# Optimization experiments

Measured on AMD Instinct MI355X. Metric: run time of the kernel, lower is better.

The kernel has to match this reference:

```python
import jax, jax.numpy as jnp
import numpy as np

N = 50000        # nodes
E = 800000       # edges
F_IN = 128       # dataset.num_features (== dim*heads so all conv layers share in_channels)
DIM = 32         # mParams['dim']
HEADS = 4        # mParams['num_heads']
HC = DIM * HEADS # 128
DEPTH = 2        # mParams['c_depth'] -> total conv layers = DEPTH + 1 = 3
L = DEPTH + 1
DIM2 = 16        # ceil(DIM/2)
NCLS = 6
SLOPE = 0.2      # GATv2Conv default negative_slope


def setup_inputs() -> dict:
    key = jax.random.key(0)
    ks = jax.random.split(key, 20)
    def lin(k, fan_in, shape):
        return jax.random.normal(k, shape, dtype=jnp.float32) / np.sqrt(fan_in)
    x = jax.random.normal(ks[0], (N, F_IN), dtype=jnp.float32)
    edge_index = jax.random.randint(ks[1], (2, E), 0, N, dtype=jnp.int64)
    batch = jnp.zeros((N,), dtype=jnp.int64)
    # stacked GATv2Conv params (all layers have in_channels = 128)
    Wl = lin(ks[2], F_IN, (L, F_IN, HC))   # lin_l weight (source transform)
    Wr = lin(ks[3], F_IN, (L, F_IN, HC))   # lin_r weight (target transform)
    bl = jnp.zeros((L, HC), dtype=jnp.float32)
    br = jnp.zeros((L, HC), dtype=jnp.float32)
    att = lin(ks[4], DIM, (L, HEADS, DIM)) # attention vector a
    cb = jnp.zeros((L, HC), dtype=jnp.float32)  # conv output bias
    W1 = lin(ks[5], HC, (HC, DIM));   b1 = jnp.zeros((DIM,), jnp.float32)
    W2 = lin(ks[6], DIM, (DIM, DIM2)); b2 = jnp.zeros((DIM2,), jnp.float32)
    W3 = lin(ks[7], 2 * DIM2, (2 * DIM2, NCLS)); b3 = jnp.zeros((NCLS,), jnp.float32)
    return {"x": x, "edge_index": edge_index, "batch": batch,
            "Wl": Wl, "Wr": Wr, "bl": bl, "br": br, "att": att, "cb": cb,
            "W1": W1, "b1": b1, "W2": W2, "b2": b2, "W3": W3, "b3": b3}


def _gatv2_layer(h, src, dst, Wl, Wr, bl, br, att, cb):
    # h: [N, F]; src/dst: [Ea] (self-loops included)
    xl = (h @ Wl + bl).reshape(N, HEADS, DIM)  # source-side transform
    xr = (h @ Wr + br).reshape(N, HEADS, DIM)  # target-side transform
    msg = xl[src] + xr[dst]                    # [Ea, H, C]
    e = jnp.where(msg > 0, msg, SLOPE * msg)   # leaky_relu
    score = jnp.einsum('ehc,hc->eh', e, att)   # [Ea, H]
    # scatter-softmax over destination nodes
    m = jax.ops.segment_max(score, dst, num_segments=N)        # [N, H]
    ex = jnp.exp(score - m[dst])
    s = jax.ops.segment_sum(ex, dst, num_segments=N)           # [N, H]
    alpha = ex / (s[dst] + 1e-16)                              # [Ea, H]
    out = jax.ops.segment_sum(alpha[:, :, None] * xl[src], dst, num_segments=N)
    return out.reshape(N, HC) + cb


def reference(x, edge_index, batch, Wl, Wr, bl, br, att, cb, W1, b1, W2, b2, W3, b3):
    src0, dst0 = edge_index[0], edge_index[1]
    loop = jnp.arange(N, dtype=edge_index.dtype)
    src = jnp.concatenate([src0, loop])  # GATv2Conv add_self_loops=True
    dst = jnp.concatenate([dst0, loop])
    h = x
    for i in range(L):
        h = jax.nn.relu(_gatv2_layer(h, src, dst, Wl[i], Wr[i], bl[i], br[i], att[i], cb[i]))
    h = jax.nn.relu(h @ W1 + b1)
    h = jax.nn.relu(h @ W2 + b2)
    # dropout(p=0.5) is identity in eval mode
    e = jnp.concatenate([h[src0], h[dst0]], axis=1)  # [E, 2*DIM2]
    out = e @ W3 + b3                                # [E, NCLS]
    return (out, e)
```

## Files before the change

kernel.cpp:

```cpp
#include <hip/hip_runtime.h>
#include <hip/hip_bf16.h>

typedef __hip_bfloat16 bf16;
typedef __attribute__((ext_vector_type(8))) short bf16x8;
typedef __attribute__((ext_vector_type(4))) float f32x4;

#define N_NODES 50000
#define E_EDGES 800000
#define EA (E_EDGES + N_NODES)
#define HC 128
#define HEADS 4
#define DIM 32
#define DIM2 16
#define NCLS 6
#define SLOPE 0.2f
#define XN (N_NODES * HC)
#define GM 32
#define HSTRIDE 152
#define WSWZ_L 32768
#define NCHUNK ((N_NODES + 1023) / 1024)

#define P_CVTI (2 * E_EDGES)
#define P_PRM  6390
#define P_WSWZ (3 * WSWZ_L)
#define P_TOT  (P_CVTI + P_PRM + P_WSWZ)

__device__ __forceinline__ float b2f(bf16 v) { return __bfloat162float(v); }
__device__ __forceinline__ unsigned short f2bfu(float f) {
    bf16 b = __float2bfloat16(f);
    return *(unsigned short*)&b;
}
__device__ __forceinline__ unsigned packbf(float a, float b) {
    return (unsigned)f2bfu(a) | ((unsigned)f2bfu(b) << 16);
}

__device__ __forceinline__ void block_detect(const void* wptr, const void* eptr,
                                             int* det, int& isf32, int& is64) {
    int tid = threadIdx.x;
    if (tid == 0) { det[0] = 0; det[1] = 0; }
    __syncthreads();
    const unsigned short* w = (const unsigned short*)wptr;
    int badf = 0;
    for (int i = tid; i < 1024; i += 256) {
        unsigned v = w[i];
        unsigned ex = (v >> 7) & 0xFF;
        if (v != 0 && (ex < 90 || ex > 150)) badf++;
    }
    const int* ei = (const int*)eptr;
    int nz = 0;
    for (int i = tid; i < 1024; i += 256) {
        if (ei[2 * i + 1] != 0) nz++;
    }
    if (badf) atomicAdd(&det[0], badf);
    if (nz)   atomicAdd(&det[1], nz);
    __syncthreads();
    isf32 = det[0] > 100;
    is64  = det[1] < 100;
}

__global__ __launch_bounds__(256) void k_prep(
        const void* eraw, const void* sWl, const void* sWr,
        const void* sbl, const void* sbr, const void* satt, const void* scb,
        const void* sW1, const void* sb1, const void* sW2, const void* sb2,
        const void* sW3, const void* sb3,
        int* __restrict__ eidx, int* __restrict__ off,
        float* __restrict__ prm, unsigned short* __restrict__ wswz) {
    __shared__ int det[2];
    int isf32, is64;
    block_detect(sWl, eraw, det, isf32, is64);

    int i = blockIdx.x * 256 + threadIdx.x;
    if (i < P_CVTI) {
        int v = is64 ? (int)((const long long*)eraw)[i] : ((const int*)eraw)[i];
        if (v < 0) v = 0;
        if (v >= N_NODES) v = N_NODES - 1;
        eidx[i] = v;
        if (i >= E_EDGES) atomicAdd(&off[v], 1);
        return;
    }
    i -= P_CVTI;
    if (i < P_PRM) {
        int j = i + 98304;
        const void* src; float* dst; int o;
        if      (j < 98688)  { src = sbl;  dst = prm + 98304;  o = j - 98304; }
        else if (j < 99072)  { src = sbr;  dst = prm + 98688;  o = j - 98688; }
        else if (j < 99456)  { src = satt; dst = prm + 99072;  o = j - 99072; }
        else if (j < 99840)  { src = scb;  dst = prm + 99456;  o = j - 99456; }
        else if (j < 103936) { src = sW1;  dst = prm + 99840;  o = j - 99840; }
        else if (j < 103968) { src = sb1;  dst = prm + 103936; o = j - 103936; }
        else if (j < 104480) { src = sW2;  dst = prm + 103968; o = j - 103968; }
        else if (j < 104496) { src = sb2;  dst = prm + 104480; o = j - 104480; }
        else if (j < 104688) { src = sW3;  dst = prm + 104496; o = j - 104496; }
        else                 { src = sb3;  dst = prm + 104688; o = j - 104688; }
        dst[o] = isf32 ? ((const float*)src)[o] : b2f(((const bf16*)src)[o]);
        return;
    }
    i -= P_PRM;
    if (i >= P_WSWZ) return;
    int L = i / WSWZ_L;
    int e = i % WSWZ_L;
    int ntile = e >> 11;
    int r2 = e & 2047;
    int ks = r2 >> 9;
    int r3 = r2 & 511;
    int lane = r3 >> 3;
    int j = r3 & 7;
    int col = ntile * 16 + (lane & 15);
    int k = ks * 32 + (lane >> 4) * 8 + j;
    const void* src = (col < HC) ? sWl : sWr;
    int idx = L * HC * HC + k * HC + (col & (HC - 1));
    float v = isf32 ? ((const float*)src)[idx] : b2f(((const bf16*)src)[idx]);
    wswz[i] = f2bfu(v);
}

__global__ __launch_bounds__(1024) void k_scan1(int* __restrict__ off, int* __restrict__ part) {
    __shared__ int s[1024];
    int tid = threadIdx.x;
    int i = blockIdx.x * 1024 + tid;
    int v = (i < N_NODES) ? off[i] + 1 : 0;
    s[tid] = v;
    __syncthreads();
    for (int o = 1; o < 1024; o <<= 1) {
        int t = (tid >= o) ? s[tid - o] : 0;
        __syncthreads();
        s[tid] += t;
        __syncthreads();
    }
    if (i < N_NODES) off[i] = s[tid] - v;
    if (tid == 1023) part[blockIdx.x] = s[1023];
}

__global__ __launch_bounds__(1024) void k_scan3(int* __restrict__ off, const int* __restrict__ part) {
    __shared__ int sbase;
    int tid = threadIdx.x;
    if (tid < 64) {
        int v = (tid < NCHUNK && tid < (int)blockIdx.x) ? part[tid] : 0;
        for (int o = 32; o > 0; o >>= 1) v += __shfl_down(v, o);
        if (tid == 0) sbase = v;
    }
    __syncthreads();
    int i = blockIdx.x * 1024 + tid;
    if (i < N_NODES) off[i] += sbase;
    if (i == 0) off[N_NODES] = EA;
}

__global__ void k_scatter(const int* __restrict__ eidx, const int* __restrict__ off,
                          int* __restrict__ fill, int* __restrict__ csrsrc) {
    int e = blockIdx.x * blockDim.x + threadIdx.x;
    if (e >= EA) return;
    int src, dst;
    if (e < E_EDGES) { src = eidx[e]; dst = eidx[E_EDGES + e]; }
    else             { src = dst = e - E_EDGES; }
    int pos = off[dst] + atomicAdd(&fill[dst], 1);
    if (pos >= 0 && pos < EA) csrsrc[pos] = src;
}

__global__ __launch_bounds__(256) void k_gemm_mfma(
        const void* __restrict__ hsrc, const void* wdet, const void* edet,
        int detect_in,
        const unsigned short* __restrict__ wswz,
        const float* __restrict__ bl, const float* __restrict__ br,
        unsigned* __restrict__ xlbf, float* __restrict__ xr) {
    __shared__ unsigned short hs[GM * HSTRIDE];
    __shared__ int det[2];
    int tid = threadIdx.x;
    int wave = tid >> 6, lane = tid & 63;
    long row0 = (long)blockIdx.x * GM;

    int f32in = 0;
    if (detect_in) {
        int is64d;
        block_detect(wdet, edet, det, f32in, is64d);
    }

    if (f32in) {
        for (int idx = tid; idx < GM * 64; idx += 256) {
            int r = idx >> 6, cp = idx & 63;
            float v0 = 0.f, v1 = 0.f;
            if (row0 + r < N_NODES) {
                const float2 hv = ((const float2*)((const float*)hsrc + (row0 + r) * HC))[cp];
                v0 = hv.x; v1 = hv.y;
            }
            *(unsigned*)&hs[r * HSTRIDE + cp * 2] = packbf(v0, v1);
        }
    } else {
        for (int idx = tid; idx < GM * 64; idx += 256) {
            int r = idx >> 6, cp = idx & 63;
            unsigned u = 0;
            if (row0 + r < N_NODES)
                u = ((const unsigned*)hsrc)[(row0 + r) * (HC / 2) + cp];
            *(unsigned*)&hs[r * HSTRIDE + cp * 2] = u;
        }
    }
    __syncthreads();

    int q = lane >> 4, l16 = lane & 15;
    for (int nt = 0; nt < 4; nt++) {
        int colbase = wave * 64 + nt * 16;
        int col = colbase + l16;
        int ntile = colbase >> 4;
        f32x4 acc0 = {0.f, 0.f, 0.f, 0.f};
        f32x4 acc1 = {0.f, 0.f, 0.f, 0.f};
#pragma unroll
        for (int ks = 0; ks < 4; ks++) {
            bf16x8 bfrag = *(const bf16x8*)(wswz + (((ntile * 4 + ks) * 64 + lane) << 3));
            bf16x8 a0 = *(const bf16x8*)(hs + l16 * HSTRIDE + ks * 32 + q * 8);
            bf16x8 a1 = *(const bf16x8*)(hs + (16 + l16) * HSTRIDE + ks * 32 + q * 8);
            acc0 = __builtin_amdgcn_mfma_f32_16x16x32_bf16(a0, bfrag, acc0, 0, 0, 0);
            acc1 = __builtin_amdgcn_mfma_f32_16x16x32_bf16(a1, bfrag, acc1, 0, 0, 0);
        }
        if (col < HC) {
            float bias = bl[col];
#pragma unroll
            for (int reg = 0; reg < 4; reg++) {
                float v0 = acc0[reg] + bias;
                float v1 = acc1[reg] + bias;
                float p0 = __shfl_xor(v0, 1);
                float p1 = __shfl_xor(v1, 1);
                if ((lane & 1) == 0) {
                    long n0 = row0 + q * 4 + reg;
                    long n1 = row0 + 16 + q * 4 + reg;
                    unsigned u0 = packbf(v0, p0);
                    unsigned u1 = packbf(v1, p1);
                    int cp = col >> 1;
                    if (n0 < N_NODES) xlbf[n0 * (HC / 2) + cp] = u0;
                    if (n1 < N_NODES) xlbf[n1 * (HC / 2) + cp] = u1;
                }
            }
        } else {
            int c = col - HC;
            float bias = br[c];
#pragma unroll
            for (int reg = 0; reg < 4; reg++) {
                long n0 = row0 + q * 4 + reg;
                long n1 = row0 + 16 + q * 4 + reg;
                if (n0 < N_NODES) xr[n0 * HC + c] = acc0[reg] + bias;
                if (n1 < N_NODES) xr[n1 * HC + c] = acc1[reg] + bias;
            }
        }
    }
}

__global__ __launch_bounds__(256) void k_attn(
        const unsigned* __restrict__ xlbf, const float* __restrict__ xr,
        const int* __restrict__ off, const int* __restrict__ csrsrc,
        const float* __restrict__ att, const float* __restrict__ cb,
        void* __restrict__ hout, int out_bf16) {
    int wave = threadIdx.x >> 6;
    int lane = threadIdx.x & 63;
    int node = blockIdx.x * 4 + wave;
    if (node >= N_NODES) return;
    int grp = lane >> 4;
    int gl  = lane & 15;
    int fb  = gl * 8;
    int head = fb >> 5;

    const float4* xrp = (const float4*)(xr + (long)node * HC + fb);
    float4 xa = xrp[0], xb = xrp[1];
    const float4* ap = (const float4*)(att + head * DIM + (fb & 31));
    float4 aa = ap[0], ab = ap[1];

    int e0 = off[node], e1 = off[node + 1];
    if (e0 < 0) e0 = 0;
    if (e1 > EA) e1 = EA;
    if (e1 <= e0) {
        if (grp == 0) {
            if (out_bf16) {
                uint4 z = {0u, 0u, 0u, 0u};
                *(uint4*)((unsigned*)hout + (long)node * (HC / 2) + gl * 4) = z;
            } else {
                float4 z = make_float4(0.f, 0.f, 0.f, 0.f);
                ((float4*)((float*)hout + (long)node * HC + fb))[0] = z;
                ((float4*)((float*)hout + (long)node * HC + fb))[1] = z;
            }
        }
        return;
    }
    int klast = e1 - 1;
    const char* xlb = (const char*)xlbf;
    unsigned glo = (unsigned)gl * 16u;
#define XLD(s) (*(const uint4*)(xlb + (((unsigned)(s) << 8) + glo)))
#define CLMP(x) ((x) < klast ? (x) : klast)

    int k0 = e0 + grp;
    int sa = csrsrc[CLMP(k0)];
    int sb = csrsrc[CLMP(k0 + 4)];
    int sc = csrsrc[CLMP(k0 + 8)];
    int sd = csrsrc[CLMP(k0 + 12)];
    int sP = csrsrc[CLMP(k0 + 16)];
    uint4 u0 = XLD(sa);
    uint4 u1 = XLD(sb);
    uint4 u2 = XLD(sc);
    uint4 u3 = XLD(sd);

    float m = -1e30f, ssum = 0.f;
    float acc[8];
#pragma unroll
    for (int j = 0; j < 8; j++) acc[j] = 0.f;

    for (int kk = k0; kk < e1; kk += 4) {
        uint4 cur = u0;
        u0 = u1; u1 = u2; u2 = u3;
        u3 = XLD(sP);
        sP = csrsrc[CLMP(kk + 20)];

        float x0 = __uint_as_float(cur.x << 16);
        float x1 = __uint_as_float(cur.x & 0xffff0000u);
        float x2 = __uint_as_float(cur.y << 16);
        float x3 = __uint_as_float(cur.y & 0xffff0000u);
        float x4 = __uint_as_float(cur.z << 16);
        float x5 = __uint_as_float(cur.z & 0xffff0000u);
        float x6 = __uint_as_float(cur.w << 16);
        float x7 = __uint_as_float(cur.w & 0xffff0000u);
        float m0 = x0 + xa.x, m1 = x1 + xa.y, m2 = x2 + xa.z, m3 = x3 + xa.w;
        float m4 = x4 + xb.x, m5 = x5 + xb.y, m6 = x6 + xb.z, m7 = x7 + xb.w;
        float l0 = fmaxf(m0, SLOPE * m0), l1 = fmaxf(m1, SLOPE * m1);
        float l2 = fmaxf(m2, SLOPE * m2), l3 = fmaxf(m3, SLOPE * m3);
        float l4 = fmaxf(m4, SLOPE * m4), l5 = fmaxf(m5, SLOPE * m5);
        float l6 = fmaxf(m6, SLOPE * m6), l7 = fmaxf(m7, SLOPE * m7);
        float p = l0 * aa.x + l1 * aa.y + l2 * aa.z + l3 * aa.w
                + l4 * ab.x + l5 * ab.y + l6 * ab.z + l7 * ab.w;
        p += __shfl_xor(p, 1);
        p += __shfl_xor(p, 2);
        float mn = fmaxf(m, p);
        float sc_ = __expf(m - mn);
        float ex = __expf(p - mn);
        ssum = ssum * sc_ + ex;
        acc[0] = acc[0] * sc_ + ex * x0;
        acc[1] = acc[1] * sc_ + ex * x1;
        acc[2] = acc[2] * sc_ + ex * x2;
        acc[3] = acc[3] * sc_ + ex * x3;
        acc[4] = acc[4] * sc_ + ex * x4;
        acc[5] = acc[5] * sc_ + ex * x5;
        acc[6] = acc[6] * sc_ + ex * x6;
        acc[7] = acc[7] * sc_ + ex * x7;
        m = mn;
    }
#undef XLD
#undef CLMP

#pragma unroll
    for (int d = 16; d <= 32; d <<= 1) {
        float mo = __shfl_xor(m, d);
        float so = __shfl_xor(ssum, d);
        float ao[8];
#pragma unroll
        for (int j = 0; j < 8; j++) ao[j] = __shfl_xor(acc[j], d);
        float mn = fmaxf(m, mo);
        float s1f = __expf(m - mn);
        float s2f = __expf(mo - mn);
        ssum = ssum * s1f + so * s2f;
#pragma unroll
        for (int j = 0; j < 8; j++) acc[j] = acc[j] * s1f + ao[j] * s2f;
        m = mn;
    }

    if (grp == 0) {
        float inv = 1.f / (ssum + 1e-16f);
        const float4* cbp = (const float4*)(cb + fb);
        float4 c0 = cbp[0], c1 = cbp[1];
        float o0 = fmaxf(acc[0] * inv + c0.x, 0.f);
        float o1 = fmaxf(acc[1] * inv + c0.y, 0.f);
        float o2 = fmaxf(acc[2] * inv + c0.z, 0.f);
        float o3 = fmaxf(acc[3] * inv + c0.w, 0.f);
        float o4 = fmaxf(acc[4] * inv + c1.x, 0.f);
        float o5 = fmaxf(acc[5] * inv + c1.y, 0.f);
        float o6 = fmaxf(acc[6] * inv + c1.z, 0.f);
        float o7 = fmaxf(acc[7] * inv + c1.w, 0.f);
        if (out_bf16) {
            uint4 w;
            w.x = packbf(o0, o1);
            w.y = packbf(o2, o3);
            w.z = packbf(o4, o5);
            w.w = packbf(o6, o7);
            *(uint4*)((unsigned*)hout + (long)node * (HC / 2) + gl * 4) = w;
        } else {
            float4 a0 = make_float4(o0, o1, o2, o3);
            float4 a1 = make_float4(o4, o5, o6, o7);
            float4* op = (float4*)((float*)hout + (long)node * HC + fb);
            op[0] = a0;
            op[1] = a1;
        }
    }
}

__global__ __launch_bounds__(256) void k_mlp(
        const float* __restrict__ h, const float* __restrict__ W1,
        const float* __restrict__ b1, const float* __restrict__ W2,
        const float* __restrict__ b2, float* __restrict__ h3) {
    __shared__ float w1s[HC * DIM];
    __shared__ float hs[16 * HC];
    __shared__ float h2s[16 * DIM];
    __shared__ float w2s[DIM * DIM2];
    int tid = threadIdx.x;
    long row0 = (long)blockIdx.x * 16;
    for (int idx = tid; idx < HC * DIM; idx += 256) w1s[idx] = W1[idx];
    for (int idx = tid; idx < DIM * DIM2; idx += 256) w2s[idx] = W2[idx];
    for (int idx = tid; idx < 16 * HC; idx += 256) {
        long g = row0 * HC + idx;
        hs[idx] = (g < (long)N_NODES * HC) ? h[g] : 0.f;
    }
    __syncthreads();
#pragma unroll
    for (int p = 0; p < 2; p++) {
        int idx = tid + p * 256;
        int r = idx >> 5, c = idx & 31;
        float acc = b1[c];
        for (int k = 0; k < HC; k++) acc += hs[r * HC + k] * w1s[k * DIM + c];
        h2s[r * DIM + c] = acc > 0.f ? acc : 0.f;
    }
    __syncthreads();
    int r = tid >> 4, c = tid & 15;
    float acc = b2[c];
    for (int k = 0; k < DIM; k++) acc += h2s[r * DIM + k] * w2s[k * DIM2 + c];
    long row = row0 + r;
    if (row < N_NODES) h3[row * DIM2 + c] = acc > 0.f ? acc : 0.f;
}

__global__ __launch_bounds__(256) void k_out(
        const float* __restrict__ h3, const int* __restrict__ eidx,
        const float* __restrict__ W3, const float* __restrict__ b3,
        void* __restrict__ dout, const void* wdet, const void* edet) {
    __shared__ float w3s[2 * DIM2 * NCLS];
    __shared__ float bs[NCLS];
    __shared__ int det[2];
    int isf32, is64d;
    block_detect(wdet, edet, det, isf32, is64d);
    int tid = threadIdx.x;
    if (tid < 2 * DIM2 * NCLS) w3s[tid] = W3[tid];
    if (tid < NCLS) bs[tid] = b3[tid];
    __syncthreads();
    int idx = blockIdx.x * 256 + tid;
    int e = idx >> 1, half = idx & 1;
    int node = eidx[half * E_EDGES + e];
    float4 t0, t1, t2, t3;
    {
        const float4* ps = (const float4*)(h3 + (long)node * DIM2);
        t0 = ps[0]; t1 = ps[1]; t2 = ps[2]; t3 = ps[3];
    }
    float v[DIM2];
    v[0] = t0.x;  v[1] = t0.y;  v[2] = t0.z;  v[3] = t0.w;
    v[4] = t1.x;  v[5] = t1.y;  v[6] = t1.z;  v[7] = t1.w;
    v[8] = t2.x;  v[9] = t2.y;  v[10] = t2.z; v[11] = t2.w;
    v[12] = t3.x; v[13] = t3.y; v[14] = t3.z; v[15] = t3.w;
    const float* wrow = w3s + half * DIM2 * NCLS;
    float o[NCLS];
#pragma unroll
    for (int j = 0; j < NCLS; j++) {
        float acc = half ? 0.f : bs[j];
#pragma unroll
        for (int k = 0; k < DIM2; k++) acc += v[k] * wrow[k * NCLS + j];
        o[j] = acc;
    }
#pragma unroll
    for (int j = 0; j < NCLS; j++) o[j] += __shfl_xor(o[j], 1);
    if (isf32) {
        float4* eo = (float4*)((float*)dout + (long)E_EDGES * NCLS
                               + (long)e * 32 + half * 16);
        eo[0] = t0; eo[1] = t1; eo[2] = t2; eo[3] = t3;
        if (!half) {
            float2* out0 = (float2*)dout;
            out0[(long)e * 3 + 0] = make_float2(o[0], o[1]);
            out0[(long)e * 3 + 1] = make_float2(o[2], o[3]);
            out0[(long)e * 3 + 2] = make_float2(o[4], o[5]);
        }
    } else {
        uint4 wa, wb;
        wa.x = packbf(v[0], v[1]);   wa.y = packbf(v[2], v[3]);
        wa.z = packbf(v[4], v[5]);   wa.w = packbf(v[6], v[7]);
        wb.x = packbf(v[8], v[9]);   wb.y = packbf(v[10], v[11]);
        wb.z = packbf(v[12], v[13]); wb.w = packbf(v[14], v[15]);
        uint4* eo = (uint4*)((bf16*)dout + (long)E_EDGES * NCLS)
                    + (long)e * 4 + half * 2;
        eo[0] = wa; eo[1] = wb;
        if (!half) {
            unsigned* out0 = (unsigned*)dout;
            out0[(long)e * 3 + 0] = packbf(o[0], o[1]);
            out0[(long)e * 3 + 1] = packbf(o[2], o[3]);
            out0[(long)e * 3 + 2] = packbf(o[4], o[5]);
        }
    }
}

extern "C" void kernel_launch(void* const* d_in, const int* in_sizes, int n_in,
                              void* d_out, int out_size, void* d_ws, size_t ws_size,
                              hipStream_t stream) {
    float* wsf   = (float*)d_ws;
    float* h     = wsf + 16;
    float* xl    = h  + (long)N_NODES * HC;
    float* xr    = xl + (long)N_NODES * HC;
    float* prm   = xr + (long)N_NODES * HC;
    unsigned short* wswz = (unsigned short*)(prm + 110000);
    int*   eidx  = (int*)(wswz + P_WSWZ);
    int*   off   = eidx + 2 * E_EDGES;
    int*   fill  = off + (N_NODES + 1);
    int*   csr   = fill + N_NODES;
    int*   part  = csr + EA;
    unsigned* xlbf = (unsigned*)xl;
    float* h3 = xl;

    float* pbl = prm + 98304;
    float* pbr = prm + 98688;
    float* patt= prm + 99072;
    float* pcb = prm + 99456;
    float* pW1 = prm + 99840;
    float* pb1 = prm + 103936;
    float* pW2 = prm + 103968;
    float* pb2 = prm + 104480;
    float* pW3 = prm + 104496;
    float* pb3 = prm + 104688;

    hipMemsetAsync(off, 0, (size_t)(2 * N_NODES + 1) * sizeof(int), stream);

    k_prep<<<(P_TOT + 255) / 256, 256, 0, stream>>>(
        d_in[1], d_in[3], d_in[4], d_in[5], d_in[6], d_in[7], d_in[8],
        d_in[9], d_in[10], d_in[11], d_in[12], d_in[13], d_in[14],
        eidx, off, prm, wswz);

    k_scan1<<<NCHUNK, 1024, 0, stream>>>(off, part);
    k_scan3<<<NCHUNK, 1024, 0, stream>>>(off, part);
    k_scatter<<<(EA + 255) / 256, 256, 0, stream>>>(eidx, off, fill, csr);

    for (int i = 0; i < 3; i++) {
        k_gemm_mfma<<<(N_NODES + GM - 1) / GM, 256, 0, stream>>>(
            i == 0 ? (const void*)d_in[0] : (const void*)h,
            d_in[3], d_in[1], i == 0 ? 1 : 0,
            wswz + (long)i * WSWZ_L, pbl + (long)i * HC, pbr + (long)i * HC,
            xlbf, xr);
        k_attn<<<(N_NODES + 3) / 4, 256, 0, stream>>>(
            xlbf, xr, off, csr, patt + (long)i * HEADS * DIM, pcb + (long)i * HC,
            (void*)h, i < 2 ? 1 : 0);
    }

    k_mlp<<<(N_NODES + 15) / 16, 256, 0, stream>>>(h, pW1, pb1, pW2, pb2, h3);

    k_out<<<(2 * E_EDGES + 255) / 256, 256, 0, stream>>>(h3, eidx, pW3, pb3, d_out,
                                                         d_in[3], d_in[1]);
}
```

Before: 608.3 us.

## Split attention per head with head-major bf16 source features

The GEMM now writes the bf16 source-side features in a head-major layout ([head][node][32]), and the attention kernel gives each wave one (head, node) pair instead of a whole node. Each lane handles two channels, and a 64-byte row is gathered per edge, so one head's gather footprint is a quarter of the full row. This launches four times as many waves and re-reads the CSR offsets and indices once per head. Those extra index loads and the extra shuffle reductions may outweigh the smaller per-wave register footprint and the higher parallelism.

```diff
diff --git a/kernel.cpp b/kernel.cpp
--- a/kernel.cpp
+++ b/kernel.cpp
@@ -211,6 +211,8 @@
         }
         if (col < HC) {
             float bias = bl[col];
+            int head = col >> 5;
+            int pair = (col >> 1) & 15;
 #pragma unroll
             for (int reg = 0; reg < 4; reg++) {
                 float v0 = acc0[reg] + bias;
@@ -222,9 +224,8 @@
                     long n1 = row0 + 16 + q * 4 + reg;
                     unsigned u0 = packbf(v0, p0);
                     unsigned u1 = packbf(v1, p1);
-                    int cp = col >> 1;
-                    if (n0 < N_NODES) xlbf[n0 * (HC / 2) + cp] = u0;
-                    if (n1 < N_NODES) xlbf[n1 * (HC / 2) + cp] = u1;
+                    if (n0 < N_NODES) xlbf[((long)head * N_NODES + n0) * 16 + pair] = u0;
+                    if (n1 < N_NODES) xlbf[((long)head * N_NODES + n1) * 16 + pair] = u1;
                 }
             }
         } else {
@@ -248,38 +249,30 @@
         void* __restrict__ hout, int out_bf16) {
     int wave = threadIdx.x >> 6;
     int lane = threadIdx.x & 63;
-    int node = blockIdx.x * 4 + wave;
-    if (node >= N_NODES) return;
+    int unit = blockIdx.x * 4 + wave;
+    int head = unit / N_NODES;
+    int node = unit - head * N_NODES;
     int grp = lane >> 4;
     int gl  = lane & 15;
-    int fb  = gl * 8;
-    int head = fb >> 5;
-
-    const float4* xrp = (const float4*)(xr + (long)node * HC + fb);
-    float4 xa = xrp[0], xb = xrp[1];
-    const float4* ap = (const float4*)(att + head * DIM + (fb & 31));
-    float4 aa = ap[0], ab = ap[1];
+
+    float2 xv = *(const float2*)(xr + (long)node * HC + head * DIM + gl * 2);
+    float2 av = *(const float2*)(att + head * DIM + gl * 2);
 
     int e0 = off[node], e1 = off[node + 1];
     if (e0 < 0) e0 = 0;
     if (e1 > EA) e1 = EA;
     if (e1 <= e0) {
         if (grp == 0) {
-            if (out_bf16) {
-                uint4 z = {0u, 0u, 0u, 0u};
-                *(uint4*)((unsigned*)hout + (long)node * (HC / 2) + gl * 4) = z;
-            } else {
-                float4 z = make_float4(0.f, 0.f, 0.f, 0.f);
-                ((float4*)((float*)hout + (long)node * HC + fb))[0] = z;
-                ((float4*)((float*)hout + (long)node * HC + fb))[1] = z;
-            }
+            if (out_bf16) ((unsigned*)hout)[(long)node * (HC / 2) + head * 16 + gl] = 0u;
+            else *(float2*)((float*)hout + (long)node * HC + head * DIM + gl * 2)
+                     = make_float2(0.f, 0.f);
         }
         return;
     }
     int klast = e1 - 1;
-    const char* xlb = (const char*)xlbf;
-    unsigned glo = (unsigned)gl * 16u;
-#define XLD(s) (*(const uint4*)(xlb + (((unsigned)(s) << 8) + glo)))
+    const char* xlb = (const char*)(xlbf + (long)head * N_NODES * 16);
+    unsigned glo = (unsigned)gl * 4u;
+#define XLD(s) (*(const unsigned*)(xlb + (((unsigned)(s) << 6) + glo)))
 #define CLMP(x) ((x) < klast ? (x) : klast)
 
     int k0 = e0 + grp;
@@ -288,52 +281,35 @@
     int sc = csrsrc[CLMP(k0 + 8)];
     int sd = csrsrc[CLMP(k0 + 12)];
     int sP = csrsrc[CLMP(k0 + 16)];
-    uint4 u0 = XLD(sa);
-    uint4 u1 = XLD(sb);
-    uint4 u2 = XLD(sc);
-    uint4 u3 = XLD(sd);
+    unsigned u0 = XLD(sa);
+    unsigned u1 = XLD(sb);
+    unsigned u2 = XLD(sc);
+    unsigned u3 = XLD(sd);
 
     float m = -1e30f, ssum = 0.f;
-    float acc[8];
-#pragma unroll
-    for (int j = 0; j < 8; j++) acc[j] = 0.f;
+    float a0 = 0.f, a1 = 0.f;
 
     for (int kk = k0; kk < e1; kk += 4) {
-        uint4 cur = u0;
+        unsigned cur = u0;
         u0 = u1; u1 = u2; u2 = u3;
         u3 = XLD(sP);
         sP = csrsrc[CLMP(kk + 20)];
 
-        float x0 = __uint_as_float(cur.x << 16);
-        float x1 = __uint_as_float(cur.x & 0xffff0000u);
-        float x2 = __uint_as_float(cur.y << 16);
-        float x3 = __uint_as_float(cur.y & 0xffff0000u);
-        float x4 = __uint_as_float(cur.z << 16);
-        float x5 = __uint_as_float(cur.z & 0xffff0000u);
-        float x6 = __uint_as_float(cur.w << 16);
-        float x7 = __uint_as_float(cur.w & 0xffff0000u);
-        float m0 = x0 + xa.x, m1 = x1 + xa.y, m2 = x2 + xa.z, m3 = x3 + xa.w;
-        float m4 = x4 + xb.x, m5 = x5 + xb.y, m6 = x6 + xb.z, m7 = x7 + xb.w;
+        float x0 = __uint_as_float(cur << 16);
+        float x1 = __uint_as_float(cur & 0xffff0000u);
+        float m0 = x0 + xv.x, m1 = x1 + xv.y;
         float l0 = fmaxf(m0, SLOPE * m0), l1 = fmaxf(m1, SLOPE * m1);
-        float l2 = fmaxf(m2, SLOPE * m2), l3 = fmaxf(m3, SLOPE * m3);
-        float l4 = fmaxf(m4, SLOPE * m4), l5 = fmaxf(m5, SLOPE * m5);
-        float l6 = fmaxf(m6, SLOPE * m6), l7 = fmaxf(m7, SLOPE * m7);
-        float p = l0 * aa.x + l1 * aa.y + l2 * aa.z + l3 * aa.w
-                + l4 * ab.x + l5 * ab.y + l6 * ab.z + l7 * ab.w;
+        float p = l0 * av.x + l1 * av.y;
         p += __shfl_xor(p, 1);
         p += __shfl_xor(p, 2);
+        p += __shfl_xor(p, 4);
+        p += __shfl_xor(p, 8);
         float mn = fmaxf(m, p);
         float sc_ = __expf(m - mn);
         float ex = __expf(p - mn);
         ssum = ssum * sc_ + ex;
-        acc[0] = acc[0] * sc_ + ex * x0;
-        acc[1] = acc[1] * sc_ + ex * x1;
-        acc[2] = acc[2] * sc_ + ex * x2;
-        acc[3] = acc[3] * sc_ + ex * x3;
-        acc[4] = acc[4] * sc_ + ex * x4;
-        acc[5] = acc[5] * sc_ + ex * x5;
-        acc[6] = acc[6] * sc_ + ex * x6;
-        acc[7] = acc[7] * sc_ + ex * x7;
+        a0 = a0 * sc_ + ex * x0;
+        a1 = a1 * sc_ + ex * x1;
         m = mn;
     }
 #undef XLD
@@ -343,43 +319,27 @@
     for (int d = 16; d <= 32; d <<= 1) {
         float mo = __shfl_xor(m, d);
         float so = __shfl_xor(ssum, d);
-        float ao[8];
-#pragma unroll
-        for (int j = 0; j < 8; j++) ao[j] = __shfl_xor(acc[j], d);
+        float b0 = __shfl_xor(a0, d);
+        float b1 = __shfl_xor(a1, d);
         float mn = fmaxf(m, mo);
         float s1f = __expf(m - mn);
         float s2f = __expf(mo - mn);
         ssum = ssum * s1f + so * s2f;
-#pragma unroll
-        for (int j = 0; j < 8; j++) acc[j] = acc[j] * s1f + ao[j] * s2f;
+        a0 = a0 * s1f + b0 * s2f;
+        a1 = a1 * s1f + b1 * s2f;
         m = mn;
     }
 
     if (grp == 0) {
         float inv = 1.f / (ssum + 1e-16f);
-        const float4* cbp = (const float4*)(cb + fb);
-        float4 c0 = cbp[0], c1 = cbp[1];
-        float o0 = fmaxf(acc[0] * inv + c0.x, 0.f);
-        float o1 = fmaxf(acc[1] * inv + c0.y, 0.f);
-        float o2 = fmaxf(acc[2] * inv + c0.z, 0.f);
-        float o3 = fmaxf(acc[3] * inv + c0.w, 0.f);
-        float o4 = fmaxf(acc[4] * inv + c1.x, 0.f);
-        float o5 = fmaxf(acc[5] * inv + c1.y, 0.f);
-        float o6 = fmaxf(acc[6] * inv + c1.z, 0.f);
-        float o7 = fmaxf(acc[7] * inv + c1.w, 0.f);
+        float2 cv = *(const float2*)(cb + head * DIM + gl * 2);
+        float o0 = fmaxf(a0 * inv + cv.x, 0.f);
+        float o1 = fmaxf(a1 * inv + cv.y, 0.f);
         if (out_bf16) {
-            uint4 w;
-            w.x = packbf(o0, o1);
-            w.y = packbf(o2, o3);
-            w.z = packbf(o4, o5);
-            w.w = packbf(o6, o7);
-            *(uint4*)((unsigned*)hout + (long)node * (HC / 2) + gl * 4) = w;
+            ((unsigned*)hout)[(long)node * (HC / 2) + head * 16 + gl] = packbf(o0, o1);
         } else {
-            float4 a0 = make_float4(o0, o1, o2, o3);
-            float4 a1 = make_float4(o4, o5, o6, o7);
-            float4* op = (float4*)((float*)hout + (long)node * HC + fb);
-            op[0] = a0;
-            op[1] = a1;
+            *(float2*)((float*)hout + (long)node * HC + head * DIM + gl * 2)
+                = make_float2(o0, o1);
         }
     }
 }
@@ -527,7 +487,7 @@
             d_in[3], d_in[1], i == 0 ? 1 : 0,
             wswz + (long)i * WSWZ_L, pbl + (long)i * HC, pbr + (long)i * HC,
             xlbf, xr);
-        k_attn<<<(N_NODES + 3) / 4, 256, 0, stream>>>(
+        k_attn<<<(N_NODES * HEADS) / 4, 256, 0, stream>>>(
             xlbf, xr, off, csr, patt + (long)i * HEADS * DIM, pcb + (long)i * HC,
             (void*)h, i < 2 ? 1 : 0);
     }
```

Result: slower. 817.4 us (+34.4%).
